# Kernel tuning notes

Hardware: AMD Instinct MI355X
Metric: run time of the kernel (lower is better)

The kernel has to match this reference:

```python
import jax, jax.numpy as jnp
import numpy as np
import math

S = 128
EPS = 1e-05

def _rope_seq(x):
    # x: [B, L, 2, s]; rope over dim=1 (sequence), matching torch rope(x, dim=1)
    B, L, two, s = x.shape
    half = s // 2
    pos = jnp.arange(L, dtype=jnp.float32)[:, None]              # [L,1] (one unsqueeze)
    inv_freq = 10000.0 ** (jnp.arange(half, dtype=jnp.float32) / half)
    sinusoid = pos[..., None] * inv_freq[None, None, :]          # [L,1,half]
    sin = jnp.sin(sinusoid)
    cos = jnp.cos(sinusoid)
    x1, x2 = jnp.split(x, 2, axis=-1)
    return jnp.concatenate([x1 * cos - x2 * sin, x2 * cos + x1 * sin], axis=-1)

def setup_inputs() -> dict:
    key = jax.random.key(0)
    ks = jax.random.split(key, 8)
    B, L, D = 8, 1024, 1024
    E = 2 * D
    x = jax.random.normal(ks[0], (B, L, D), dtype=jnp.float32)
    g = jnp.ones((1,), dtype=jnp.float32)
    uv_w = jax.random.normal(ks[1], (2 * E + S, D), dtype=jnp.float32) * 0.02
    gamma = jax.random.uniform(ks[2], (2, S), dtype=jnp.float32)
    beta = jax.random.uniform(ks[3], (2, S), dtype=jnp.float32)
    w_rel = jax.random.uniform(ks[4], (2 * L - 1,), dtype=jnp.float32)
    o_w = jax.random.normal(ks[5], (D, E), dtype=jnp.float32) * 0.02
    res_scale = jnp.ones((D,), dtype=jnp.float32)
    return {"x": x, "g": g, "uv_w": uv_w, "gamma": gamma, "beta": beta,
            "w_rel": w_rel, "o_w": o_w, "res_scale": res_scale}

def reference(x, g, uv_w, gamma, beta, w_rel, o_w, res_scale):
    B, L, D = x.shape
    E = (uv_w.shape[0] - S) // 2
    sqrt_s = math.sqrt(S)
    # ScaleNorm
    norm = jnp.linalg.norm(x, axis=-1, keepdims=True) * (D ** -0.5)
    xn = x / jnp.maximum(norm, EPS) * g
    # gated projection + activation
    uv = jax.nn.silu(xn @ uv_w.T)                               # [B,L,2E+S]
    u = uv[..., :E]
    v = uv[..., E:2 * E]
    base = uv[..., 2 * E:]                                       # [B,L,S]
    base = base[:, :, None, :] * gamma[None, None] + beta        # [B,L,2,S]
    base = _rope_seq(base)
    q = base[:, :, 0]                                            # [B,L,S]
    k = base[:, :, 1]
    qk = jnp.einsum('bis,bjs->bij', q, k)                        # [B,L,L]
    # Toeplitz relative bias: bias[i,j] = w_rel[j - i + L - 1]
    idx = jnp.arange(L)[None, :] - jnp.arange(L)[:, None] + (L - 1)
    qk = qk + w_rel[idx][None]
    kernel = jnp.square(jax.nn.relu(qk / sqrt_s))
    out = u * jnp.einsum('bij,bje->bie', kernel, v)              # [B,L,E]
    out = out @ o_w.T                                            # [B,L,D]
    return x * res_scale + out
```

## Files before the change

### kernel.cpp

```cpp
#include <hip/hip_runtime.h>
#include <hip/hip_bf16.h>
#include <math.h>


typedef __hip_bfloat16 bf16;
using v8s = __attribute__((ext_vector_type(8))) short;
using v4f = __attribute__((ext_vector_type(4))) float;
typedef unsigned short u16;

#define BTCH 8
#define LSEQ 1024
#define DDIM 1024
#define EDIM 2048
#define SDIM 128
#define UVN  4224
#define SLABW 4096
#define BUFW  (4 * SLABW)

__device__ __forceinline__ float ldany(const void* p, size_t i, int bf) {
  return bf ? __bfloat162float(((const bf16*)p)[i]) : ((const float*)p)[i];
}
__device__ __forceinline__ void stany(void* p, size_t i, float v, int bf) {
  if (bf) ((bf16*)p)[i] = __float2bfloat16(v);
  else    ((float*)p)[i] = v;
}
__device__ __forceinline__ u16 f2bf(float x) {
  bf16 b = __float2bfloat16(x);
  return *reinterpret_cast<u16*>(&b);
}
__device__ __forceinline__ float bf2f(u16 u) {
  return __uint_as_float((unsigned)u << 16);
}
__device__ __forceinline__ float silu(float v) {
  return v / (1.0f + __expf(-v));
}

__device__ __forceinline__ void gld16(const u16* g, u16* l) {
  __builtin_amdgcn_global_load_lds(
      (const __attribute__((address_space(1))) void*)g,
      (__attribute__((address_space(3))) void*)l, 16, 0, 0);
}

__device__ __forceinline__ const v8s* swz_rd(const u16* slab, int row, int q) {
  return (const v8s*)(slab + row * 32 + ((q ^ ((row >> 1) & 3)) << 3));
}

__global__ void detect_kernel(const u16* g16, int* flag) {
  *flag = (g16[0] == 0x3F80) ? 1 : 0;
}

__global__ __launch_bounds__(256) void wsplit_kernel(const void* __restrict__ w,
                                                     u16* __restrict__ whi,
                                                     u16* __restrict__ wlo,
                                                     const int* __restrict__ flagp,
                                                     int n) {
  const int bf = *flagp;
  const size_t i = ((size_t)blockIdx.x * 256 + threadIdx.x) * 8;
  if (i >= (size_t)n) return;
  if (bf) {
    *(uint4*)(whi + i) = *(const uint4*)((const u16*)w + i);
  } else {
    const float* wf = (const float*)w;
    float t[8];
    *(float4*)&t[0] = *(const float4*)(wf + i);
    *(float4*)&t[4] = *(const float4*)(wf + i + 4);
    u16 h[8], l[8];
    #pragma unroll
    for (int j = 0; j < 8; j++) {
      h[j] = f2bf(t[j]);
      l[j] = f2bf(t[j] - bf2f(h[j]));
    }
    *(uint4*)(whi + i) = *(uint4*)&h[0];
    *(uint4*)(wlo + i) = *(uint4*)&l[0];
  }
}

__global__ __launch_bounds__(256) void rmsnorm_kernel(const void* __restrict__ x,
                                                      const void* __restrict__ g,
                                                      u16* __restrict__ xnhi,
                                                      u16* __restrict__ xnlo,
                                                      const int* __restrict__ flagp,
                                                      unsigned long long row0) {
  const int bf = *flagp;
  const int m = blockIdx.x;
  const size_t gbase = (row0 + m) * DDIM;
  float ss = 0.f;
  float vals[4];
  #pragma unroll
  for (int i = 0; i < 4; i++) {
    vals[i] = ldany(x, gbase + threadIdx.x + i * 256, bf);
    ss += vals[i] * vals[i];
  }
  #pragma unroll
  for (int o = 32; o > 0; o >>= 1) ss += __shfl_down(ss, o);
  __shared__ float red[5];
  if ((threadIdx.x & 63) == 0) red[threadIdx.x >> 6] = ss;
  __syncthreads();
  if (threadIdx.x == 0) {
    float tot = red[0] + red[1] + red[2] + red[3];
    float rms = sqrtf(tot * (1.0f / DDIM));
    red[4] = ldany(g, 0, bf) / fmaxf(rms, 1e-5f);
  }
  __syncthreads();
  const float scale = red[4];
  #pragma unroll
  for (int i = 0; i < 4; i++) {
    const size_t idx = (size_t)m * DDIM + threadIdx.x + i * 256;
    float v = vals[i] * scale;
    u16 h = f2bf(v);
    xnhi[idx] = h;
    xnlo[idx] = f2bf(v - bf2f(h));
  }
}

__device__ __forceinline__ void mfma_core(u16* __restrict__ sm,
                                          const u16* __restrict__ AhiG,
                                          const u16* __restrict__ AloG, int lda,
                                          const u16* __restrict__ BhiG,
                                          const u16* __restrict__ BloG, int ldb,
                                          int use_blo, int K, v4f acc[4][4]) {
  const int tid = threadIdx.x;
  const int w = tid >> 6, lane = tid & 63, quad = lane >> 4, lr = lane & 15;
  const int wr = w >> 1, wc = w & 1;
  const int sr0 = w * 16 + (lane >> 2);
  const int sch = lane & 3;

  auto stage = [&](int buf, int kk) {
    u16* lbase = sm + buf * BUFW + w * 512;
    #pragma unroll
    for (int c = 0; c < 2; c++) {
      const int r = sr0 + c * 64;
      const int sc = sch ^ ((r >> 1) & 3);
      u16* ld = lbase + c * 2048;
      const size_t oa = (size_t)r * lda + kk + sc * 8;
      const size_t ob = (size_t)r * ldb + kk + sc * 8;
      gld16(AhiG + oa, ld);
      gld16(AloG + oa, ld + SLABW);
      gld16(BhiG + ob, ld + 2 * SLABW);
      if (use_blo) gld16(BloG + ob, ld + 3 * SLABW);
    }
  };

  stage(0, 0);
  int cur = 0;
  for (int k0 = 0; k0 < K; k0 += 32) {
    __syncthreads();
    if (k0 + 32 < K) stage(cur ^ 1, k0 + 32);
    const u16* sA = sm + cur * BUFW;
    v8s aH[4], aL[4];
    #pragma unroll
    for (int rt = 0; rt < 4; rt++) {
      const int row = wr * 64 + rt * 16 + lr;
      aH[rt] = *swz_rd(sA, row, quad);
      aL[rt] = *swz_rd(sA + SLABW, row, quad);
    }
    #pragma unroll
    for (int ct = 0; ct < 4; ct++) {
      const int brow = wc * 64 + ct * 16 + lr;
      const v8s bh = *swz_rd(sA + 2 * SLABW, brow, quad);
      #pragma unroll
      for (int rt = 0; rt < 4; rt++)
        acc[rt][ct] = __builtin_amdgcn_mfma_f32_16x16x32_bf16(aH[rt], bh, acc[rt][ct], 0, 0, 0);
      #pragma unroll
      for (int rt = 0; rt < 4; rt++)
        acc[rt][ct] = __builtin_amdgcn_mfma_f32_16x16x32_bf16(aL[rt], bh, acc[rt][ct], 0, 0, 0);
      if (use_blo) {
        const v8s bl = *swz_rd(sA + 3 * SLABW, brow, quad);
        #pragma unroll
        for (int rt = 0; rt < 4; rt++)
          acc[rt][ct] = __builtin_amdgcn_mfma_f32_16x16x32_bf16(aH[rt], bl, acc[rt][ct], 0, 0, 0);
      }
    }
    cur ^= 1;
  }
  __syncthreads();
}

template <typename F>
__device__ __forceinline__ void epilogue_rows(const v4f acc[4][4], F body) {
  const int tid = threadIdx.x;
  const int w = tid >> 6, lane = tid & 63;
  const int quad = lane >> 4, lr = lane & 15;
  const int wr = w >> 1, wc = w & 1;
  #pragma unroll
  for (int rt = 0; rt < 4; rt++)
    #pragma unroll
    for (int rg = 0; rg < 4; rg++) {
      const int lrow = wr * 64 + rt * 16 + quad * 4 + rg;
      #pragma unroll
      for (int ct = 0; ct < 4; ct++) {
        const int lcol = wc * 64 + ct * 16 + lr;
        body(lrow, lcol, acc[rt][ct][rg]);
      }
    }
}

__global__ __launch_bounds__(256) void gemm_uv_kernel(const u16* __restrict__ xnhi,
                                                      const u16* __restrict__ xnlo,
                                                      const u16* __restrict__ uvwhi,
                                                      const u16* __restrict__ uvwlo,
                                                      float* __restrict__ u,
                                                      u16* __restrict__ vThi,
                                                      u16* __restrict__ vTlo,
                                                      float* __restrict__ base,
                                                      const int* __restrict__ flagp) {
  __shared__ __align__(16) u16 sm[2 * BUFW];
  const int bf = *flagp;
  const int bm = blockIdx.y * 128, bn = blockIdx.x * 128;
  v4f acc[4][4];
  #pragma unroll
  for (int rt = 0; rt < 4; rt++)
    #pragma unroll
    for (int ct = 0; ct < 4; ct++) acc[rt][ct] = (v4f){0.f, 0.f, 0.f, 0.f};
  mfma_core(sm, xnhi + (size_t)bm * DDIM, xnlo + (size_t)bm * DDIM, DDIM,
            uvwhi + (size_t)bn * DDIM, uvwlo + (size_t)bn * DDIM, DDIM,
            bf ? 0 : 1, DDIM, acc);

  if (bn < EDIM) {
    epilogue_rows(acc, [&](int lrow, int lcol, float av) {
      u[(size_t)(bm + lrow) * EDIM + bn + lcol] = silu(av);
    });
  } else if (bn < 2 * EDIM) {
    const int z = bm >> 10, l0 = bm & (LSEQ - 1), e0 = bn - EDIM;
    const int tid = threadIdx.x;
    #pragma unroll
    for (int pass = 0; pass < 2; pass++) {
      __syncthreads();
      epilogue_rows(acc, [&](int lrow, int lcol, float av) {
        const float v = silu(av);
        const u16 hh = f2bf(v);
        sm[lcol * 136 + lrow] = pass ? f2bf(v - bf2f(hh)) : hh;
      });
      __syncthreads();
      u16* dst = pass ? vTlo : vThi;
      const int c = tid >> 1, part = tid & 1;
      const uint4* srcp = (const uint4*)(sm + c * 136 + part * 64);
      uint4* dstp = (uint4*)(dst + ((size_t)z * EDIM + e0 + c) * LSEQ + l0 + part * 64);
      #pragma unroll
      for (int j = 0; j < 8; j++) dstp[j] = srcp[j];
    }
  } else {
    epilogue_rows(acc, [&](int lrow, int lcol, float av) {
      base[(size_t)(bm + lrow) * SDIM + (bn - 2 * EDIM) + lcol] = silu(av);
    });
  }
}

__global__ __launch_bounds__(64) void rope_kernel(const float* __restrict__ base,
                                                  const void* __restrict__ gamma,
                                                  const void* __restrict__ beta,
                                                  u16* __restrict__ qhi,
                                                  u16* __restrict__ qlo,
                                                  u16* __restrict__ khi,
                                                  u16* __restrict__ klo,
                                                  const int* __restrict__ flagp) {
  const int bf = *flagp;
  const int m = blockIdx.x;
  const int pos = m & (LSEQ - 1);
  const int j = threadIdx.x;
  double f = pow(10000.0, (double)j / 64.0);
  double ds, dc;
  sincos((double)pos * f, &ds, &dc);
  const float s = (float)ds, c = (float)dc;
  const float b1 = base[(size_t)m * SDIM + j];
  const float b2 = base[(size_t)m * SDIM + 64 + j];
  {
    float x1 = b1 * ldany(gamma, j, bf) + ldany(beta, j, bf);
    float x2 = b2 * ldany(gamma, 64 + j, bf) + ldany(beta, 64 + j, bf);
    float o1 = x1 * c - x2 * s, o2 = x2 * c + x1 * s;
    u16 h1 = f2bf(o1), h2 = f2bf(o2);
    qhi[(size_t)m * SDIM + j] = h1;      qlo[(size_t)m * SDIM + j] = f2bf(o1 - bf2f(h1));
    qhi[(size_t)m * SDIM + 64 + j] = h2; qlo[(size_t)m * SDIM + 64 + j] = f2bf(o2 - bf2f(h2));
  }
  {
    float x1 = b1 * ldany(gamma, SDIM + j, bf) + ldany(beta, SDIM + j, bf);
    float x2 = b2 * ldany(gamma, SDIM + 64 + j, bf) + ldany(beta, SDIM + 64 + j, bf);
    float o1 = x1 * c - x2 * s, o2 = x2 * c + x1 * s;
    u16 h1 = f2bf(o1), h2 = f2bf(o2);
    khi[(size_t)m * SDIM + j] = h1;      klo[(size_t)m * SDIM + j] = f2bf(o1 - bf2f(h1));
    khi[(size_t)m * SDIM + 64 + j] = h2; klo[(size_t)m * SDIM + 64 + j] = f2bf(o2 - bf2f(h2));
  }
}

__global__ __launch_bounds__(256) void gemm_qk_kernel(const u16* __restrict__ qhi,
                                                      const u16* __restrict__ qlo,
                                                      const u16* __restrict__ khi,
                                                      const u16* __restrict__ klo,
                                                      const void* __restrict__ w_rel,
                                                      u16* __restrict__ kerhi,
                                                      u16* __restrict__ kerlo,
                                                      const int* __restrict__ flagp) {
  __shared__ __align__(16) u16 sm[2 * BUFW];
  const int bf = *flagp;
  const int z = blockIdx.z;
  const int bm = blockIdx.y * 128, bn = blockIdx.x * 128;
  v4f acc[4][4];
  #pragma unroll
  for (int rt = 0; rt < 4; rt++)
    #pragma unroll
    for (int ct = 0; ct < 4; ct++) acc[rt][ct] = (v4f){0.f, 0.f, 0.f, 0.f};
  const size_t ao = ((size_t)z * LSEQ + bm) * SDIM;
  const size_t bo = ((size_t)z * LSEQ + bn) * SDIM;
  mfma_core(sm, qhi + ao, qlo + ao, SDIM, khi + bo, klo + bo, SDIM, 1, SDIM, acc);
  const float inv_sqrt_s = 0.08838834764831845f;
  epilogue_rows(acc, [&](int lrow, int lcol, float av) {
    const int gi = bm + lrow, gj = bn + lcol;
    float v = av + ldany(w_rel, gj - gi + (LSEQ - 1), bf);
    v = fmaxf(v, 0.f) * inv_sqrt_s;
    v = v * v;
    const u16 hh = f2bf(v);
    const size_t idx = ((size_t)z * LSEQ + gi) * LSEQ + gj;
    kerhi[idx] = hh;
    kerlo[idx] = f2bf(v - bf2f(hh));
  });
}

__global__ __launch_bounds__(256) void gemm_av_kernel(const u16* __restrict__ kerhi,
                                                      const u16* __restrict__ kerlo,
                                                      const u16* __restrict__ vThi,
                                                      const u16* __restrict__ vTlo,
                                                      const float* __restrict__ u,
                                                      u16* __restrict__ out2hi,
                                                      u16* __restrict__ out2lo) {
  __shared__ __align__(16) u16 sm[2 * BUFW];
  const int z = blockIdx.z;
  const int bm = blockIdx.y * 128, bn = blockIdx.x * 128;
  v4f acc[4][4];
  #pragma unroll
  for (int rt = 0; rt < 4; rt++)
    #pragma unroll
    for (int ct = 0; ct < 4; ct++) acc[rt][ct] = (v4f){0.f, 0.f, 0.f, 0.f};
  const size_t ao = ((size_t)z * LSEQ + bm) * LSEQ;
  const size_t bo = ((size_t)z * EDIM + bn) * LSEQ;
  mfma_core(sm, kerhi + ao, kerlo + ao, LSEQ, vThi + bo, vTlo + bo, LSEQ,
            1, LSEQ, acc);
  epilogue_rows(acc, [&](int lrow, int lcol, float av) {
    const size_t grow = (size_t)z * LSEQ + bm + lrow;
    const float v = av * u[grow * EDIM + bn + lcol];
    const u16 hh = f2bf(v);
    out2hi[grow * EDIM + bn + lcol] = hh;
    out2lo[grow * EDIM + bn + lcol] = f2bf(v - bf2f(hh));
  });
}

__global__ __launch_bounds__(256) void gemm_out_kernel(const u16* __restrict__ out2hi,
                                                       const u16* __restrict__ out2lo,
                                                       const u16* __restrict__ owhi,
                                                       const u16* __restrict__ owlo,
                                                       const void* __restrict__ x,
                                                       const void* __restrict__ res_scale,
                                                       void* __restrict__ out,
                                                       const int* __restrict__ flagp,
                                                       unsigned long long row0) {
  __shared__ __align__(16) u16 sm[2 * BUFW];
  const int bf = *flagp;
  const int bm = blockIdx.y * 128, bn = blockIdx.x * 128;
  v4f acc[4][4];
  #pragma unroll
  for (int rt = 0; rt < 4; rt++)
    #pragma unroll
    for (int ct = 0; ct < 4; ct++) acc[rt][ct] = (v4f){0.f, 0.f, 0.f, 0.f};
  mfma_core(sm, out2hi + (size_t)bm * EDIM, out2lo + (size_t)bm * EDIM, EDIM,
            owhi + (size_t)bn * EDIM, owlo + (size_t)bn * EDIM, EDIM,
            bf ? 0 : 1, EDIM, acc);
  epilogue_rows(acc, [&](int lrow, int lcol, float av) {
    const size_t gidx = (row0 + bm + lrow) * DDIM + bn + lcol;
    float v = av + ldany(x, gidx, bf) * ldany(res_scale, bn + lcol, bf);
    stany(out, gidx, v, bf);
  });
}

extern "C" void kernel_launch(void* const* d_in, const int* in_sizes, int n_in,
                              void* d_out, int out_size, void* d_ws, size_t ws_size,
                              hipStream_t stream) {
  const void* x         = d_in[0];
  const void* g         = d_in[1];
  const void* uv_w      = d_in[2];
  const void* gamma     = d_in[3];
  const void* beta      = d_in[4];
  const void* w_rel     = d_in[5];
  const void* o_w       = d_in[6];
  const void* res_scale = d_in[7];

  char* ws = (char*)d_ws;
  size_t off = 0;
  int* flag = (int*)(ws + off); off += 256;
  u16* uvwhi = (u16*)(ws + off); off += (size_t)UVN * DDIM * 2;
  u16* uvwlo = (u16*)(ws + off); off += (size_t)UVN * DDIM * 2;
  u16* owhi  = (u16*)(ws + off); off += (size_t)DDIM * EDIM * 2;
  u16* owlo  = (u16*)(ws + off); off += (size_t)DDIM * EDIM * 2;

  int nb = 1;
  for (int cand = 8; cand >= 1; cand >>= 1) {
    size_t need = off + (size_t)cand * 35127296ULL;
    if (ws_size >= need) { nb = cand; break; }
  }
  const int rows = nb * LSEQ;

  u16*   xnhi = (u16*)(ws + off); off += (size_t)rows * DDIM * 2;
  u16*   xnlo = (u16*)(ws + off); off += (size_t)rows * DDIM * 2;
  float* u    = (float*)(ws + off); off += (size_t)rows * EDIM * 4;
  float* base = (float*)(ws + off); off += (size_t)rows * SDIM * 4;
  u16*   qhi  = (u16*)(ws + off); off += (size_t)rows * SDIM * 2;
  u16*   qlo  = (u16*)(ws + off); off += (size_t)rows * SDIM * 2;
  u16*   khi  = (u16*)(ws + off); off += (size_t)rows * SDIM * 2;
  u16*   klo  = (u16*)(ws + off); off += (size_t)rows * SDIM * 2;
  u16*   kerhi= (u16*)(ws + off); off += (size_t)nb * LSEQ * LSEQ * 2;
  u16*   kerlo= (u16*)(ws + off); off += (size_t)nb * LSEQ * LSEQ * 2;
  u16*   vThi = (u16*)(ws + off); off += (size_t)nb * EDIM * LSEQ * 2;
  u16*   vTlo = (u16*)(ws + off); off += (size_t)nb * EDIM * LSEQ * 2;
  u16*   o2hi = (u16*)(ws + off); off += (size_t)rows * EDIM * 2;
  u16*   o2lo = (u16*)(ws + off); off += (size_t)rows * EDIM * 2;

  detect_kernel<<<1, 1, 0, stream>>>((const u16*)g, flag);
  wsplit_kernel<<<(UVN * DDIM) / (8 * 256), 256, 0, stream>>>(uv_w, uvwhi, uvwlo,
                                                              flag, UVN * DDIM);
  wsplit_kernel<<<(DDIM * EDIM) / (8 * 256), 256, 0, stream>>>(o_w, owhi, owlo,
                                                               flag, DDIM * EDIM);

  for (int b = 0; b < BTCH / nb; b++) {
    const unsigned long long row0 = (unsigned long long)b * rows;

    rmsnorm_kernel<<<rows, 256, 0, stream>>>(x, g, xnhi, xnlo, flag, row0);
    {
      dim3 grid(UVN / 128, rows / 128);
      gemm_uv_kernel<<<grid, 256, 0, stream>>>(xnhi, xnlo, uvwhi, uvwlo, u,
                                               vThi, vTlo, base, flag);
    }
    rope_kernel<<<rows, 64, 0, stream>>>(base, gamma, beta, qhi, qlo, khi, klo, flag);
    {
      dim3 grid(LSEQ / 128, LSEQ / 128, nb);
      gemm_qk_kernel<<<grid, 256, 0, stream>>>(qhi, qlo, khi, klo, w_rel,
                                               kerhi, kerlo, flag);
    }
    {
      dim3 grid(EDIM / 128, LSEQ / 128, nb);
      gemm_av_kernel<<<grid, 256, 0, stream>>>(kerhi, kerlo, vThi, vTlo, u,
                                               o2hi, o2lo);
    }
    {
      dim3 grid(DDIM / 128, rows / 128);
      gemm_out_kernel<<<grid, 256, 0, stream>>>(o2hi, o2lo, owhi, owlo, x,
                                                res_scale, d_out, flag, row0);
    }
  }
}
```

Baseline: 716.6 us.

## Single-buffer LDS in GEMM core, loading fragments to registers before next stage

Replaces the double-buffered LDS staging in the shared MFMA GEMM core with a single buffer. Each iteration now reads all A and B fragments into registers, synchronises, issues the async global-to-LDS loads for the next K slice, then runs the MFMAs and synchronises again. This halves shared-memory use per block (a fixed size is kept for the uv kernel, likely because its epilogue needs more space), which should allow more resident blocks per CU. The cost is a second barrier per iteration and more live vector registers for the B fragments.

```diff
diff --git a/kernel.cpp b/kernel.cpp
--- a/kernel.cpp
+++ b/kernel.cpp
@@ -124,9 +124,13 @@
   const int wr = w >> 1, wc = w & 1;
   const int sr0 = w * 16 + (lane >> 2);
   const int sch = lane & 3;
-
-  auto stage = [&](int buf, int kk) {
-    u16* lbase = sm + buf * BUFW + w * 512;
+  u16* sAhi = sm;
+  u16* sAlo = sm + SLABW;
+  u16* sBhi = sm + 2 * SLABW;
+  u16* sBlo = sm + 3 * SLABW;
+
+  auto stage = [&](int kk) {
+    u16* lbase = sm + w * 512;
     #pragma unroll
     for (int c = 0; c < 2; c++) {
       const int r = sr0 + c * 64;
@@ -141,39 +145,40 @@
     }
   };
 
-  stage(0, 0);
-  int cur = 0;
+  stage(0);
+  __syncthreads();
   for (int k0 = 0; k0 < K; k0 += 32) {
-    __syncthreads();
-    if (k0 + 32 < K) stage(cur ^ 1, k0 + 32);
-    const u16* sA = sm + cur * BUFW;
-    v8s aH[4], aL[4];
+    v8s aH[4], aL[4], bh[4], bl[4];
     #pragma unroll
     for (int rt = 0; rt < 4; rt++) {
       const int row = wr * 64 + rt * 16 + lr;
-      aH[rt] = *swz_rd(sA, row, quad);
-      aL[rt] = *swz_rd(sA + SLABW, row, quad);
+      aH[rt] = *swz_rd(sAhi, row, quad);
+      aL[rt] = *swz_rd(sAlo, row, quad);
     }
     #pragma unroll
     for (int ct = 0; ct < 4; ct++) {
       const int brow = wc * 64 + ct * 16 + lr;
-      const v8s bh = *swz_rd(sA + 2 * SLABW, brow, quad);
+      bh[ct] = *swz_rd(sBhi, brow, quad);
+      if (use_blo) bl[ct] = *swz_rd(sBlo, brow, quad);
+    }
+    __syncthreads();
+    if (k0 + 32 < K) stage(k0 + 32);
+    #pragma unroll
+    for (int ct = 0; ct < 4; ct++) {
       #pragma unroll
       for (int rt = 0; rt < 4; rt++)
-        acc[rt][ct] = __builtin_amdgcn_mfma_f32_16x16x32_bf16(aH[rt], bh, acc[rt][ct], 0, 0, 0);
+        acc[rt][ct] = __builtin_amdgcn_mfma_f32_16x16x32_bf16(aH[rt], bh[ct], acc[rt][ct], 0, 0, 0);
       #pragma unroll
       for (int rt = 0; rt < 4; rt++)
-        acc[rt][ct] = __builtin_amdgcn_mfma_f32_16x16x32_bf16(aL[rt], bh, acc[rt][ct], 0, 0, 0);
+        acc[rt][ct] = __builtin_amdgcn_mfma_f32_16x16x32_bf16(aL[rt], bh[ct], acc[rt][ct], 0, 0, 0);
       if (use_blo) {
-        const v8s bl = *swz_rd(sA + 3 * SLABW, brow, quad);
         #pragma unroll
         for (int rt = 0; rt < 4; rt++)
-          acc[rt][ct] = __builtin_amdgcn_mfma_f32_16x16x32_bf16(aH[rt], bl, acc[rt][ct], 0, 0, 0);
+          acc[rt][ct] = __builtin_amdgcn_mfma_f32_16x16x32_bf16(aH[rt], bl[ct], acc[rt][ct], 0, 0, 0);
       }
     }
-    cur ^= 1;
-  }
-  __syncthreads();
+    __syncthreads();
+  }
 }
 
 template <typename F>
@@ -204,7 +209,7 @@
                                                       u16* __restrict__ vTlo,
                                                       float* __restrict__ base,
                                                       const int* __restrict__ flagp) {
-  __shared__ __align__(16) u16 sm[2 * BUFW];
+  __shared__ __align__(16) u16 sm[17408];
   const int bf = *flagp;
   const int bm = blockIdx.y * 128, bn = blockIdx.x * 128;
   v4f acc[4][4];
@@ -290,7 +295,7 @@
                                                       u16* __restrict__ kerhi,
                                                       u16* __restrict__ kerlo,
                                                       const int* __restrict__ flagp) {
-  __shared__ __align__(16) u16 sm[2 * BUFW];
+  __shared__ __align__(16) u16 sm[BUFW];
   const int bf = *flagp;
   const int z = blockIdx.z;
   const int bm = blockIdx.y * 128, bn = blockIdx.x * 128;
@@ -322,7 +327,7 @@
                                                       const float* __restrict__ u,
                                                       u16* __restrict__ out2hi,
                                                       u16* __restrict__ out2lo) {
-  __shared__ __align__(16) u16 sm[2 * BUFW];
+  __shared__ __align__(16) u16 sm[BUFW];
   const int z = blockIdx.z;
   const int bm = blockIdx.y * 128, bn = blockIdx.x * 128;
   v4f acc[4][4];
@@ -352,7 +357,7 @@
                                                        void* __restrict__ out,
                                                        const int* __restrict__ flagp,
                                                        unsigned long long row0) {
-  __shared__ __align__(16) u16 sm[2 * BUFW];
+  __shared__ __align__(16) u16 sm[BUFW];
   const int bf = *flagp;
   const int bm = blockIdx.y * 128, bn = blockIdx.x * 128;
   v4f acc[4][4];
```

Result: faster. 696.7 us (-2.8%).
